# Kernel optimization log

Measured on AMD Instinct MI355X. Metric: run time of the kernel, lower is better.

## Reference

```python
import jax, jax.numpy as jnp
import numpy as np
import math

B, S, E, H = 2, 2048, 1024, 16
D = E // H  # d_head = 64

def setup_inputs() -> dict:
    key = jax.random.key(0)
    ks = jax.random.split(key, 7)
    query = jax.random.normal(ks[0], (B, S, E), dtype=jnp.float32)
    k_in = jax.random.normal(ks[1], (B, S, E), dtype=jnp.float32)
    v_in = jax.random.normal(ks[2], (B, S, E), dtype=jnp.float32)
    # causal mask, broadcastable over batch and heads; mask==0 positions are blocked
    mask = jnp.tril(jnp.ones((S, S), dtype=jnp.int32))[None, None]
    scale = 1.0 / math.sqrt(E)
    w_q = jax.random.normal(ks[3], (E, E), dtype=jnp.float32) * scale
    w_k = jax.random.normal(ks[4], (E, E), dtype=jnp.float32) * scale
    w_v = jax.random.normal(ks[5], (E, E), dtype=jnp.float32) * scale
    w_o = jax.random.normal(ks[6], (E, E), dtype=jnp.float32) * scale
    return {"query": query, "key": k_in, "value": v_in, "mask": mask,
            "w_q": w_q, "w_k": w_k, "w_v": w_v, "w_o": w_o}

def reference(query, key, value, mask, w_q, w_k, w_v, w_o):
    # projections (nn.Linear with no bias: x @ W^T); split heads -> [B,H,S,D]
    q = (query @ w_q.T).reshape(B, S, H, D).transpose(0, 2, 1, 3)
    k = (key @ w_k.T).reshape(B, S, H, D).transpose(0, 2, 1, 3)
    v = (value @ w_v.T).reshape(B, S, H, D).transpose(0, 2, 1, 3)
    # scaled dot-product scores [B,H,S,S]
    scores = jnp.einsum('bhqd,bhkd->bhqk', q, k) / math.sqrt(D)
    scores = jnp.where(mask == 0, jnp.float32(-1e9), scores)
    attn = jax.nn.softmax(scores, axis=-1)  # dropout p=0.0 -> identity
    out = jnp.einsum('bhqk,bhkd->bhqd', attn, v)  # [B,H,S,D]
    out = out.transpose(0, 2, 1, 3).reshape(B, S, E)
    return out @ w_o.T
```

## Files before the change

### kernel.cpp

```cpp
#include <hip/hip_runtime.h>
#include <hip/hip_bf16.h>

#define B_ 2
#define S_ 2048
#define E_ 1024
#define H_ 16
#define D_ 64

typedef __attribute__((ext_vector_type(8))) short bf16x8;
typedef __attribute__((ext_vector_type(4))) float f32x4;

static __device__ __forceinline__ unsigned short f2bf(float x) {
    union { float f; unsigned u; } v; v.f = x;
    unsigned r = v.u + 0x7FFF + ((v.u >> 16) & 1);
    return (unsigned short)(r >> 16);
}

static __device__ __forceinline__ unsigned pack2bf(float a, float b) {
    union { float f; unsigned u; } x, y; x.f = a; y.f = b;
    unsigned ra = x.u + 0x7FFF + ((x.u >> 16) & 1);
    unsigned rb = y.u + 0x7FFF + ((y.u >> 16) & 1);
    return (ra >> 16) | (rb & 0xFFFF0000u);
}

static __device__ __forceinline__ unsigned packtrunc(float a, float b) {
    union { float f; unsigned u; } x, y; x.f = a; y.f = b;
    return __builtin_amdgcn_perm(y.u, x.u, 0x07060302);
}

static __device__ __forceinline__ void async_copy16(const void* gsrc, void* ldst) {
    __builtin_amdgcn_global_load_lds(
        (const __attribute__((address_space(1))) void*)gsrc,
        (__attribute__((address_space(3))) void*)ldst, 16, 0, 0);
}

__global__ void cvt_all(const float* __restrict__ s0, const float* __restrict__ s1,
                        const float* __restrict__ s2, const float* __restrict__ s3,
                        const float* __restrict__ s4, const float* __restrict__ s5,
                        const float* __restrict__ s6,
                        unsigned short* __restrict__ xdst, unsigned short* __restrict__ wdst,
                        float scq) {
    int b = blockIdx.x;
    const float* src; unsigned short* dst; int i; float c = 1.f;
    if (b < 12288) {
        int ti = b >> 12, lb = b & 4095;
        src = (ti == 0) ? s0 : (ti == 1) ? s1 : s2;
        dst = xdst + (size_t)ti * 4194304;
        i = lb * 256 + threadIdx.x;
    } else {
        int r = b - 12288, ti = r >> 10, lb = r & 1023;
        src = (ti == 0) ? s3 : (ti == 1) ? s4 : (ti == 2) ? s5 : s6;
        dst = wdst + (size_t)ti * 1048576;
        i = lb * 256 + threadIdx.x;
        if (ti == 0) c = scq;
    }
    float4 f = ((const float4*)src)[i];
    ushort4 o;
    o.x = f2bf(f.x * c); o.y = f2bf(f.y * c); o.z = f2bf(f.z * c); o.w = f2bf(f.w * c);
    ((ushort4*)dst)[i] = o;
}

template <int MODE>
__global__ __launch_bounds__(256) void gemm128(
    const unsigned short* __restrict__ A0, const unsigned short* __restrict__ B0,
    void* __restrict__ C0, int M, int N, int K) {
    __shared__ __align__(16) unsigned short KV[8][4096];
    const unsigned short* A = A0;
    const unsigned short* Bm = B0;
    int z = 0;
    if (MODE == 4) {
        z = blockIdx.z;
        A  = A0 + (size_t)z * 4194304;
        Bm = B0 + (size_t)z * 1048576;
    }
    const int o = (int)(blockIdx.x + (blockIdx.y << 3));
    const int cx = o & 7, tx = o >> 3;
    const int bm = ((cx << 2) + (tx >> 3)) * 128;
    const int bn = (tx & 7) * 128;
    const int tid = threadIdx.x;
    const int w = tid >> 6, lane = tid & 63;
    const int col = lane & 15, quad = lane >> 4;
    const int wm = (w >> 1) * 64, wn = (w & 1) * 64;
    const int cq = (quad ^ ((col >> 1) & 3)) << 3;

    f32x4 acc[4][4] = {};

    const int r0 = tid >> 2;
    const int cg = (tid & 3) ^ ((r0 >> 1) & 3);
    const size_t aoff0 = (size_t)(bm + r0) * K + cg * 8;
    const size_t aoff1 = (size_t)(bm + r0 + 64) * K + cg * 8;
    const size_t boff0 = (size_t)(bn + r0) * K + cg * 8;
    const size_t boff1 = (size_t)(bn + r0 + 64) * K + cg * 8;
    const int l0 = tid * 8, l1 = (tid + 256) * 8;

    const int nk = K >> 5;

    async_copy16(A  + aoff0,      &KV[0][l0]);
    async_copy16(A  + aoff1,      &KV[0][l1]);
    async_copy16(Bm + boff0,      &KV[4][l0]);
    async_copy16(Bm + boff1,      &KV[4][l1]);
    async_copy16(A  + aoff0 + 32, &KV[1][l0]);
    async_copy16(A  + aoff1 + 32, &KV[1][l1]);
    async_copy16(Bm + boff0 + 32, &KV[5][l0]);
    async_copy16(Bm + boff1 + 32, &KV[5][l1]);

    for (int kt = 0; kt < nk; kt++) {
        {
            const int kp = kt + 2;
            const int src = (kp < nk) ? kp : (nk - 1);
            const int bp = kp & 3;
            const size_t ko = (size_t)src * 32;
            async_copy16(A  + aoff0 + ko, &KV[bp][l0]);
            async_copy16(A  + aoff1 + ko, &KV[bp][l1]);
            async_copy16(Bm + boff0 + ko, &KV[4 + bp][l0]);
            async_copy16(Bm + boff1 + ko, &KV[4 + bp][l1]);
        }
        asm volatile("s_waitcnt vmcnt(8)" ::: "memory");
        __builtin_amdgcn_s_barrier();

        const unsigned short* Ab = &KV[kt & 3][0];
        const unsigned short* Bb = &KV[4 + (kt & 3)][0];
        bf16x8 af[4], bfr[4];
#pragma unroll
        for (int i = 0; i < 4; i++) af[i]  = *(const bf16x8*)&Ab[(wm + i * 16 + col) * 32 + cq];
#pragma unroll
        for (int j = 0; j < 4; j++) bfr[j] = *(const bf16x8*)&Bb[(wn + j * 16 + col) * 32 + cq];
#pragma unroll
        for (int i = 0; i < 4; i++)
#pragma unroll
            for (int j = 0; j < 4; j++)
                acc[i][j] = __builtin_amdgcn_mfma_f32_16x16x32_bf16(af[i], bfr[j], acc[i][j], 0, 0, 0);
    }

    __syncthreads();

    if (MODE == 3) {
#pragma unroll
        for (int i = 0; i < 4; i++)
#pragma unroll
            for (int j = 0; j < 4; j++)
#pragma unroll
                for (int r = 0; r < 4; r++) {
                    int gm = bm + wm + i * 16 + quad * 4 + r;
                    int gn = bn + wn + j * 16 + col;
                    ((float*)C0)[(size_t)gm * N + gn] = acc[i][j][r];
                }
    } else {
        unsigned short* scr = &KV[w * 2][0];
        const int b  = (bm + wm) >> 11;
        const int s0 = (bm + wm) & 2047;
        const int hh = (bn + wn) >> 6;
        unsigned short* outp = (unsigned short*)C0 + (size_t)z * 4194304;
        if (z == 2) {
#pragma unroll
            for (int i = 0; i < 4; i++)
#pragma unroll
                for (int j = 0; j < 4; j++) {
                    int n = j * 16 + col;
                    int c = i * 2 + (quad >> 1);
                    uint2 pk;
                    pk.x = pack2bf(acc[i][j][0], acc[i][j][1]);
                    pk.y = pack2bf(acc[i][j][2], acc[i][j][3]);
                    *(uint2*)&scr[n * 64 + ((c ^ (n & 7)) << 3) + ((quad & 1) << 2)] = pk;
                }
#pragma unroll
            for (int it = 0; it < 8; it++) {
                int slot = it * 64 + lane, n = slot >> 3, c = slot & 7;
                uint4 v = *(uint4*)&scr[n * 64 + ((c ^ (n & 7)) << 3)];
                *(uint4*)&outp[(((size_t)b * H_ + hh) * D_ + n) * S_ + s0 + c * 8] = v;
            }
        } else {
#pragma unroll
            for (int i = 0; i < 4; i++)
#pragma unroll
                for (int j = 0; j < 4; j++)
#pragma unroll
                    for (int r = 0; r < 4; r++) {
                        int m = i * 16 + quad * 4 + r, n = j * 16 + col;
                        scr[m * 64 + (((n >> 3) ^ (m & 7)) << 3) + (n & 7)] = f2bf(acc[i][j][r]);
                    }
#pragma unroll
            for (int it = 0; it < 8; it++) {
                int slot = it * 64 + lane, m = slot >> 3, c = slot & 7;
                uint4 v = *(uint4*)&scr[m * 64 + ((c ^ (m & 7)) << 3)];
                *(uint4*)&outp[(((size_t)b * H_ + hh) * S_ + s0 + m) * (size_t)D_ + c * 8] = v;
            }
        }
    }
}

__global__ __launch_bounds__(512) void attn_kernel(
    const unsigned short* __restrict__ Q, const unsigned short* __restrict__ K_,
    const unsigned short* __restrict__ Vt, unsigned short* __restrict__ Out) {
    __shared__ __align__(16) unsigned short KV[8][4096];
    __shared__ __align__(16) float Lred[4][2][64];
    const int o = (int)(blockIdx.x + (blockIdx.y << 4));
    const int cx = o & 7, tx = o >> 3;
    const int hloc = (tx >> 1) & 3;
    const int f_ = (tx ^ (tx >> 5)) & 1;
    const int G_ = (((tx >> 4) & 1) << 2) | (((tx >> 3) & 1) << 1) | (tx & 1);
    const int qb = f_ ? (G_ ^ 15) : G_;
    const int bh = (cx << 2) + hloc;
    const int q0 = qb * 128;
    const int tid = threadIdx.x;
    const int w = tid >> 6, lane = tid & 63;
    const int qg = w >> 1, kh = w & 1, kh32 = kh << 5;
    const int col = lane & 15, quad = lane >> 4, swz = col & 7;
    const int qw0 = q0 + qg * 32;
    const float NINF = -__builtin_huge_valf();

    const unsigned short* Qh = Q + (size_t)bh * S_ * D_;
    const unsigned short* Kh = K_ + (size_t)bh * S_ * D_;
    const unsigned short* Vh = Vt + (size_t)bh * D_ * S_;

    bf16x8 qf[2][2];
#pragma unroll
    for (int i = 0; i < 2; i++)
#pragma unroll
        for (int h = 0; h < 2; h++)
            qf[i][h] = *(const bf16x8*)(Qh + (size_t)(qw0 + i * 16 + col) * 64 + h * 32 + quad * 8);

    f32x4 o_[2][4] = {};
    float lsum[2] = {0.f, 0.f};

    const int sRow = tid >> 3, sCg = (tid & 7) ^ (sRow & 7);
    const size_t koff = (size_t)sRow * 64 + sCg * 8;
    const size_t voff = (size_t)sRow * S_ + sCg * 8;
    const int ldsoff = tid * 8;

    const int nk = 2 * (qb + 1);

    async_copy16(Kh + koff, &KV[0][ldsoff]);
    async_copy16(Vh + voff, &KV[4][ldsoff]);
    async_copy16(Kh + koff + 64 * 64, &KV[1][ldsoff]);
    async_copy16(Vh + voff + 64, &KV[5][ldsoff]);

    for (int kt = 0; kt < nk; kt++) {
        const int k0 = kt * 64;
        {
            const int kp = kt + 2;
            const int src = (kp < nk) ? kp : (nk - 1);
            const int bp = kp & 3;
            async_copy16(Kh + koff + (size_t)src * 4096, &KV[bp][ldsoff]);
            async_copy16(Vh + voff + (size_t)src * 64, &KV[4 + bp][ldsoff]);
        }
        asm volatile("s_waitcnt vmcnt(4)" ::: "memory");
        __builtin_amdgcn_s_barrier();

        if (k0 + kh32 > qw0 + 31) continue;

        const unsigned short* Kb = &KV[kt & 3][0];
        const unsigned short* Vb = &KV[4 + (kt & 3)][0];

        f32x4 sc[2][2] = {};
        __builtin_amdgcn_s_setprio(1);
#pragma unroll
        for (int h = 0; h < 2; h++) {
            const int cq = ((h * 4 + quad) ^ swz) * 8;
#pragma unroll
            for (int ct = 0; ct < 2; ct++) {
                bf16x8 kf = *(const bf16x8*)&Kb[(kh32 + ct * 16 + col) * 64 + cq];
                sc[0][ct] = __builtin_amdgcn_mfma_f32_16x16x32_bf16(kf, qf[0][h], sc[0][ct], 0, 0, 0);
                sc[1][ct] = __builtin_amdgcn_mfma_f32_16x16x32_bf16(kf, qf[1][h], sc[1][ct], 0, 0, 0);
            }
        }
        __builtin_amdgcn_s_setprio(0);
        if (k0 + kh32 + 31 <= qw0) {
#pragma unroll
            for (int i = 0; i < 2; i++)
#pragma unroll
                for (int ct = 0; ct < 2; ct++) {
#pragma unroll
                    for (int r = 0; r < 4; r++)
                        sc[i][ct][r] = __builtin_amdgcn_exp2f(sc[i][ct][r]);
                    lsum[i] += (sc[i][ct][0] + sc[i][ct][1]) + (sc[i][ct][2] + sc[i][ct][3]);
                }
        } else {
#pragma unroll
            for (int i = 0; i < 2; i++)
#pragma unroll
                for (int ct = 0; ct < 2; ct++) {
#pragma unroll
                    for (int r = 0; r < 4; r++) {
                        int key = k0 + kh32 + ct * 16 + quad * 4 + r;
                        int qidx = qw0 + i * 16 + col;
                        float s = (key <= qidx) ? sc[i][ct][r] : NINF;
                        sc[i][ct][r] = __builtin_amdgcn_exp2f(s);
                    }
                    lsum[i] += (sc[i][ct][0] + sc[i][ct][1]) + (sc[i][ct][2] + sc[i][ct][3]);
                }
        }
        union { bf16x8 v; unsigned u[4]; } pf[2];
#pragma unroll
        for (int i = 0; i < 2; i++) {
            pf[i].u[0] = packtrunc(sc[i][0][0], sc[i][0][1]);
            pf[i].u[1] = packtrunc(sc[i][0][2], sc[i][0][3]);
            pf[i].u[2] = packtrunc(sc[i][1][0], sc[i][1][1]);
            pf[i].u[3] = packtrunc(sc[i][1][2], sc[i][1][3]);
        }
        __builtin_amdgcn_s_setprio(1);
#pragma unroll
        for (int dt = 0; dt < 4; dt++) {
            const int row = dt * 16 + col;
            const int ko0 = kh32 + quad * 4;
            const int ko1 = ko0 + 16;
            union { bf16x8 v; uint2 d2[2]; } vf;
            vf.d2[0] = *(const uint2*)&Vb[row * 64 + (((ko0 >> 3) ^ (row & 7)) << 3) + (ko0 & 7)];
            vf.d2[1] = *(const uint2*)&Vb[row * 64 + (((ko1 >> 3) ^ (row & 7)) << 3) + (ko1 & 7)];
#pragma unroll
            for (int i = 0; i < 2; i++)
                o_[i][dt] = __builtin_amdgcn_mfma_f32_16x16x32_bf16(vf.v, pf[i].v, o_[i][dt], 0, 0, 0);
        }
        __builtin_amdgcn_s_setprio(0);
    }

    __syncthreads();
    if (kh == 1) {
        f32x4* R = (f32x4*)&KV[0][0] + qg * 512 + lane * 8;
#pragma unroll
        for (int i = 0; i < 2; i++)
#pragma unroll
            for (int dt = 0; dt < 4; dt++) R[i * 4 + dt] = o_[i][dt];
        Lred[qg][0][lane] = lsum[0];
        Lred[qg][1][lane] = lsum[1];
    }
    __syncthreads();
    if (kh == 0) {
        f32x4* R = (f32x4*)&KV[0][0] + qg * 512 + lane * 8;
#pragma unroll
        for (int i = 0; i < 2; i++)
#pragma unroll
            for (int dt = 0; dt < 4; dt++) o_[i][dt] += R[i * 4 + dt];
        lsum[0] += Lred[qg][0][lane];
        lsum[1] += Lred[qg][1][lane];

        const int b = bh >> 4, hh = bh & 15;
#pragma unroll
        for (int i = 0; i < 2; i++) {
            float l = lsum[i];
            l += __shfl_xor(l, 16);
            l += __shfl_xor(l, 32);
            float inv = 1.f / l;
            int gq = qw0 + i * 16 + col;
#pragma unroll
            for (int dt = 0; dt < 4; dt++) {
                uint2 pk;
                pk.x = pack2bf(o_[i][dt][0] * inv, o_[i][dt][1] * inv);
                pk.y = pack2bf(o_[i][dt][2] * inv, o_[i][dt][3] * inv);
                *(uint2*)&Out[((size_t)b * S_ + gq) * E_ + hh * 64 + dt * 16 + quad * 4] = pk;
            }
        }
    }
}

extern "C" void kernel_launch(void* const* d_in, const int* in_sizes, int n_in,
                              void* d_out, int out_size, void* d_ws, size_t ws_size,
                              hipStream_t stream) {
    const float* query = (const float*)d_in[0];
    const float* key_i = (const float*)d_in[1];
    const float* value = (const float*)d_in[2];
    const float* w_q = (const float*)d_in[4];
    const float* w_k = (const float*)d_in[5];
    const float* w_v = (const float*)d_in[6];
    const float* w_o = (const float*)d_in[7];
    float* out = (float*)d_out;

    const int M = B_ * S_;
    const int N = E_, K = E_;

    char* ws = (char*)d_ws;
    unsigned short* xq  = (unsigned short*)(ws);
    unsigned short* wqb = (unsigned short*)(ws + (24u << 20));
    unsigned short* Qb  = (unsigned short*)(ws + (32u << 20));
    unsigned short* Kb  = (unsigned short*)(ws + (40u << 20));
    unsigned short* Vtb = (unsigned short*)(ws + (48u << 20));
    unsigned short* Ab  = (unsigned short*)(ws + (56u << 20));

    const float SCQ = 0.125f * 1.44269504088896f;

    cvt_all<<<16384, 256, 0, stream>>>(query, key_i, value, w_q, w_k, w_v, w_o,
                                       xq, wqb, SCQ);

    gemm128<4><<<dim3(N / 128, M / 128, 3), 256, 0, stream>>>(xq, wqb, Qb, M, N, K);

    attn_kernel<<<dim3(S_ / 128, B_ * H_), 512, 0, stream>>>(Qb, Kb, Vtb, Ab);

    gemm128<3><<<dim3(N / 128, M / 128), 256, 0, stream>>>(
        Ab, wqb + 3u * 1048576u, out, M, N, K);
}
```

Before: 207.9 us.

## Replace QKV projection GEMM with 256x256-tile, 8-wave pipelined kernel

Adds a gemm256 kernel for the batched Q/K/V projections. It uses 256x256 output tiles, 512 threads, and 128KB of LDS double-buffered via async copies, with fine-grained interleaving of staging, LDS reads and MFMA phases separated by barriers. MFMA sections get raised wave priority. The larger tiles raise arithmetic intensity and cut global traffic, and the software pipeline hides load latency. In exchange the launch has fewer blocks (192), and heavy register and LDS use may limit occupancy.

```diff
diff --git a/kernel.cpp b/kernel.cpp
--- a/kernel.cpp
+++ b/kernel.cpp
@@ -60,6 +60,128 @@
     ((ushort4*)dst)[i] = o;
 }
 
+__global__ __launch_bounds__(512, 2) void gemm256(
+    const unsigned short* __restrict__ A0, const unsigned short* __restrict__ B0,
+    void* __restrict__ C0) {
+    __shared__ __align__(16) unsigned short L[65536];
+    const int z = blockIdx.z;
+    const unsigned short* A  = A0 + (size_t)z * 4194304;
+    const unsigned short* Bm = B0 + (size_t)z * 1048576;
+    const int o = (int)(blockIdx.x + (blockIdx.y << 2));
+    const int cx = o & 7, tx = o >> 3;
+    const int bm = (cx * 2 + (tx >> 2)) * 256;
+    const int bn = (tx & 3) * 256;
+    const int tid = threadIdx.x;
+    const int w = tid >> 6, lane = tid & 63;
+    const int wr = w >> 2, wc = w & 3;
+    const int col = lane & 15, quad = lane >> 4;
+    const int r0 = tid >> 3, cg = (tid & 7) ^ (r0 & 7);
+    const size_t aR = (size_t)(bm + r0) * 1024 + cg * 8;
+    const size_t bR = (size_t)(bn + r0) * 1024 + cg * 8;
+    const int l0 = tid * 8, l1 = tid * 8 + 4096;
+    const int ach = (quad ^ (col & 7)) * 8;
+    const int aRd = wr * 8192 + col * 64 + ach;
+    const int bRd = 32768 + (wc >> 1) * 8192 + (wc & 1) * 4096 + col * 64 + ach;
+
+    f32x4 acc[8][4] = {};
+    bf16x8 bA[4][2], bB0[2][2], bB1[2][2];
+
+#define STAGE_A(d, h, t) do { \
+    async_copy16(A + aR + (size_t)((h) * 128) * 1024 + (t) * 64, &L[((d) * 2 + (h)) * 8192 + l0]); \
+    async_copy16(A + aR + (size_t)((h) * 128 + 64) * 1024 + (t) * 64, &L[((d) * 2 + (h)) * 8192 + l1]); \
+} while (0)
+#define STAGE_B(d, h, t) do { \
+    async_copy16(Bm + bR + (size_t)((h) * 128) * 1024 + (t) * 64, &L[32768 + ((d) * 2 + (h)) * 8192 + l0]); \
+    async_copy16(Bm + bR + (size_t)((h) * 128 + 64) * 1024 + (t) * 64, &L[32768 + ((d) * 2 + (h)) * 8192 + l1]); \
+} while (0)
+#define RD_A(d, mh) do { _Pragma("unroll") for (int i = 0; i < 4; i++) { \
+    bA[i][0] = *(const bf16x8*)&L[(d) * 16384 + (mh) * 4096 + i * 1024 + aRd]; \
+    bA[i][1] = *(const bf16x8*)&L[(d) * 16384 + (mh) * 4096 + i * 1024 + (aRd ^ 32)]; } } while (0)
+#define RD_B(d, nh, BB) do { _Pragma("unroll") for (int j = 0; j < 2; j++) { \
+    BB[j][0] = *(const bf16x8*)&L[(d) * 16384 + (nh) * 2048 + j * 1024 + bRd]; \
+    BB[j][1] = *(const bf16x8*)&L[(d) * 16384 + (nh) * 2048 + j * 1024 + (bRd ^ 32)]; } } while (0)
+#define MM(m0, BB, n0) do { __builtin_amdgcn_s_setprio(1); \
+    _Pragma("unroll") for (int i = 0; i < 4; i++) _Pragma("unroll") for (int j = 0; j < 2; j++) { \
+        acc[(m0) + i][(n0) + j] = __builtin_amdgcn_mfma_f32_16x16x32_bf16(bA[i][0], BB[j][0], acc[(m0) + i][(n0) + j], 0, 0, 0); \
+        acc[(m0) + i][(n0) + j] = __builtin_amdgcn_mfma_f32_16x16x32_bf16(bA[i][1], BB[j][1], acc[(m0) + i][(n0) + j], 0, 0, 0); } \
+    __builtin_amdgcn_s_setprio(0); } while (0)
+#define BARX __builtin_amdgcn_s_barrier()
+#define VMW asm volatile("s_waitcnt vmcnt(4)" ::: "memory")
+
+    STAGE_B(0, 0, 0); STAGE_B(0, 1, 0);
+    STAGE_A(0, 0, 0); STAGE_A(0, 1, 0);
+    STAGE_B(1, 0, 1); STAGE_B(1, 1, 1);
+    VMW; BARX;
+
+#pragma unroll 1
+    for (int j = 0; j < 8; j++) {
+        const int to = 2 * j + 1;
+        const int tn = (2 * j + 2 < 16) ? 2 * j + 2 : 15;
+        const int tm = (2 * j + 3 < 16) ? 2 * j + 3 : 15;
+        STAGE_A(1, 0, to); RD_A(0, 0); RD_B(0, 0, bB0); BARX; MM(0, bB0, 0); BARX;
+        STAGE_A(1, 1, to); RD_B(0, 1, bB1);             BARX; MM(0, bB1, 2); BARX;
+        STAGE_B(0, 0, tn); RD_A(0, 1);                  BARX; MM(4, bB1, 2); BARX;
+        STAGE_B(0, 1, tn);                              BARX; MM(4, bB0, 0); VMW; BARX;
+        STAGE_A(0, 0, tn); RD_A(1, 0); RD_B(1, 0, bB0); BARX; MM(0, bB0, 0); BARX;
+        STAGE_A(0, 1, tn); RD_B(1, 1, bB1);             BARX; MM(0, bB1, 2); BARX;
+        STAGE_B(1, 0, tm); RD_A(1, 1);                  BARX; MM(4, bB1, 2); BARX;
+        STAGE_B(1, 1, tm);                              BARX; MM(4, bB0, 0); VMW; BARX;
+    }
+#undef STAGE_A
+#undef STAGE_B
+#undef RD_A
+#undef RD_B
+#undef MM
+#undef BARX
+#undef VMW
+
+    __syncthreads();
+
+    unsigned short* scr = &L[w * 8192];
+    const int grow0 = bm + wr * 128;
+    const int b  = grow0 >> 11;
+    const int s0 = grow0 & 2047;
+    const int hh = (bn + wc * 64) >> 6;
+    unsigned short* outp = (unsigned short*)C0 + (size_t)z * 4194304;
+    if (z == 2) {
+#pragma unroll
+        for (int mi = 0; mi < 8; mi++)
+#pragma unroll
+            for (int nj = 0; nj < 4; nj++) {
+                int n = nj * 16 + col;
+                int c = mi * 2 + (quad >> 1);
+                uint2 pk;
+                pk.x = pack2bf(acc[mi][nj][0], acc[mi][nj][1]);
+                pk.y = pack2bf(acc[mi][nj][2], acc[mi][nj][3]);
+                *(uint2*)&scr[n * 128 + ((c ^ (n & 7)) << 3) + ((quad & 1) << 2)] = pk;
+            }
+        asm volatile("s_waitcnt lgkmcnt(0)" ::: "memory");
+#pragma unroll
+        for (int it = 0; it < 16; it++) {
+            int slot = it * 64 + lane, n = slot >> 4, c = slot & 15;
+            uint4 v = *(uint4*)&scr[n * 128 + ((c ^ (n & 7)) << 3)];
+            *(uint4*)&outp[(((size_t)b * H_ + hh) * D_ + n) * S_ + s0 + c * 8] = v;
+        }
+    } else {
+#pragma unroll
+        for (int mi = 0; mi < 8; mi++)
+#pragma unroll
+            for (int nj = 0; nj < 4; nj++)
+#pragma unroll
+                for (int r = 0; r < 4; r++) {
+                    int m = mi * 16 + quad * 4 + r, n = nj * 16 + col;
+                    scr[m * 64 + (((n >> 3) ^ (m & 7)) << 3) + (n & 7)] = f2bf(acc[mi][nj][r]);
+                }
+        asm volatile("s_waitcnt lgkmcnt(0)" ::: "memory");
+#pragma unroll
+        for (int it = 0; it < 16; it++) {
+            int slot = it * 64 + lane, m = slot >> 3, c = slot & 7;
+            uint4 v = *(uint4*)&scr[m * 64 + ((c ^ (m & 7)) << 3)];
+            *(uint4*)&outp[(((size_t)b * H_ + hh) * S_ + s0 + m) * (size_t)D_ + c * 8] = v;
+        }
+    }
+}
+
 template <int MODE>
 __global__ __launch_bounds__(256) void gemm128(
     const unsigned short* __restrict__ A0, const unsigned short* __restrict__ B0,
@@ -67,12 +189,6 @@
     __shared__ __align__(16) unsigned short KV[8][4096];
     const unsigned short* A = A0;
     const unsigned short* Bm = B0;
-    int z = 0;
-    if (MODE == 4) {
-        z = blockIdx.z;
-        A  = A0 + (size_t)z * 4194304;
-        Bm = B0 + (size_t)z * 1048576;
-    }
     const int o = (int)(blockIdx.x + (blockIdx.y << 3));
     const int cx = o & 7, tx = o >> 3;
     const int bm = ((cx << 2) + (tx >> 3)) * 128;
@@ -145,47 +261,6 @@
                     int gn = bn + wn + j * 16 + col;
                     ((float*)C0)[(size_t)gm * N + gn] = acc[i][j][r];
                 }
-    } else {
-        unsigned short* scr = &KV[w * 2][0];
-        const int b  = (bm + wm) >> 11;
-        const int s0 = (bm + wm) & 2047;
-        const int hh = (bn + wn) >> 6;
-        unsigned short* outp = (unsigned short*)C0 + (size_t)z * 4194304;
-        if (z == 2) {
-#pragma unroll
-            for (int i = 0; i < 4; i++)
-#pragma unroll
-                for (int j = 0; j < 4; j++) {
-                    int n = j * 16 + col;
-                    int c = i * 2 + (quad >> 1);
-                    uint2 pk;
-                    pk.x = pack2bf(acc[i][j][0], acc[i][j][1]);
-                    pk.y = pack2bf(acc[i][j][2], acc[i][j][3]);
-                    *(uint2*)&scr[n * 64 + ((c ^ (n & 7)) << 3) + ((quad & 1) << 2)] = pk;
-                }
-#pragma unroll
-            for (int it = 0; it < 8; it++) {
-                int slot = it * 64 + lane, n = slot >> 3, c = slot & 7;
-                uint4 v = *(uint4*)&scr[n * 64 + ((c ^ (n & 7)) << 3)];
-                *(uint4*)&outp[(((size_t)b * H_ + hh) * D_ + n) * S_ + s0 + c * 8] = v;
-            }
-        } else {
-#pragma unroll
-            for (int i = 0; i < 4; i++)
-#pragma unroll
-                for (int j = 0; j < 4; j++)
-#pragma unroll
-                    for (int r = 0; r < 4; r++) {
-                        int m = i * 16 + quad * 4 + r, n = j * 16 + col;
-                        scr[m * 64 + (((n >> 3) ^ (m & 7)) << 3) + (n & 7)] = f2bf(acc[i][j][r]);
-                    }
-#pragma unroll
-            for (int it = 0; it < 8; it++) {
-                int slot = it * 64 + lane, m = slot >> 3, c = slot & 7;
-                uint4 v = *(uint4*)&scr[m * 64 + ((c ^ (m & 7)) << 3)];
-                *(uint4*)&outp[(((size_t)b * H_ + hh) * S_ + s0 + m) * (size_t)D_ + c * 8] = v;
-            }
-        }
     }
 }
 
@@ -381,10 +456,10 @@
     cvt_all<<<16384, 256, 0, stream>>>(query, key_i, value, w_q, w_k, w_v, w_o,
                                        xq, wqb, SCQ);
 
-    gemm128<4><<<dim3(N / 128, M / 128, 3), 256, 0, stream>>>(xq, wqb, Qb, M, N, K);
+    gemm256<<<dim3(4, 16, 3), 512, 0, stream>>>(xq, wqb, Qb);
 
     attn_kernel<<<dim3(S_ / 128, B_ * H_), 512, 0, stream>>>(Qb, Kb, Vtb, Ab);
 
-    gemm128<3><<<dim3(N / 128, M / 128), 256, 0, stream>>>(
+    gemm128<3><<<dim3(8, 32), 256, 0, stream>>>(
         Ab, wqb + 3u * 1048576u, out, M, N, K);
 }
```

New measurement: 204.6 us. Within noise of the previous version (-1.6%).
